# Kernel tuning notes

Hardware: AMD Instinct MI355X
Metric: run time of the kernel (lower is better)

## Reference

```python
import jax, jax.numpy as jnp
import numpy as np

N, D, E, L, H, F1, G, A = 4096, 256, 131072, 3, 4, 128, 16, 32

def setup_inputs() -> dict:
    key = jax.random.key(0)
    ks = jax.random.split(key, 12)
    s = lambda k, shape, fan: jax.random.normal(k, shape, jnp.float32) / np.sqrt(fan)
    return {
        "x": jax.random.normal(ks[0], (N, D), jnp.float32),
        "edge_attr": jax.random.uniform(ks[1], (E,), jnp.float32),
        "conv_Wself": s(ks[2], (L, D, D), D),
        "conv_Wnbr": s(ks[3], (L, D, D), D),
        "conv_b": jnp.zeros((L, D), jnp.float32),
        "bn_gamma": jnp.ones((L - 1, D), jnp.float32),
        "bn_beta": jnp.zeros((L - 1, D), jnp.float32),
        "bn_mean": jnp.zeros((L - 1, D), jnp.float32),
        "bn_var": jnp.ones((L - 1, D), jnp.float32),
        "Wqkv": s(ks[4], (3, D, D), D),
        "bqkv": jnp.zeros((3, D), jnp.float32),
        "Wo": s(ks[5], (D, D), D),
        "bo": jnp.zeros((D,), jnp.float32),
        "fc1_W": s(ks[6], (D, F1), D),
        "fc1_b": jnp.zeros((F1,), jnp.float32),
        "AW1": s(ks[7], (G, F1, A), F1),
        "Ab1": jnp.zeros((G, A), jnp.float32),
        "AW2": s(ks[8], (G, A, 1), A),
        "Ab2": jnp.zeros((G, 1), jnp.float32),
        "edge_index": jax.random.randint(ks[9], (2, E), 0, N, jnp.int32),
        "node_groups": jax.random.randint(ks[10], (N,), 0, G, jnp.int32),
    }


def reference(x, edge_attr, conv_Wself, conv_Wnbr, conv_b, bn_gamma, bn_beta,
              bn_mean, bn_var, Wqkv, bqkv, Wo, bo, fc1_W, fc1_b,
              AW1, Ab1, AW2, Ab2, edge_index, node_groups):
    src, dst = edge_index[0], edge_index[1]
    # message-passing conv stack (edge_attr only used by the last, non-attention layer)
    for i in range(L):
        msg = x[src]
        if i == L - 1:
            msg = msg * edge_attr[:, None]
        agg = jax.ops.segment_sum(msg, dst, num_segments=N)
        x = x @ conv_Wself[i] + agg @ conv_Wnbr[i] + conv_b[i]
        if i < L - 1:
            x = bn_gamma[i] * (x - bn_mean[i]) * jax.lax.rsqrt(bn_var[i] + 1e-5) + bn_beta[i]
            x = jax.nn.elu(x)
    # hierarchy self-attention over all N nodes (batch of 1), residual add
    dh = D // H
    q = (x @ Wqkv[0] + bqkv[0]).reshape(N, H, dh)
    k = (x @ Wqkv[1] + bqkv[1]).reshape(N, H, dh)
    v = (x @ Wqkv[2] + bqkv[2]).reshape(N, H, dh)
    scores = jnp.einsum('nhd,mhd->hnm', q, k) / np.sqrt(dh).astype(np.float32)
    attn = jax.nn.softmax(scores, axis=-1)
    o = jnp.einsum('hnm,mhd->nhd', attn, v).reshape(N, D) @ Wo + bo
    x = x + o
    feats = jax.nn.elu(x @ fc1_W + fc1_b)  # [N, F1]; dropout is eval no-op
    # MoE-style per-node group adapter routing: gather tiny MLP weights per node
    h = jax.nn.relu(jnp.einsum('nd,nda->na', feats, AW1[node_groups]) + Ab1[node_groups])
    out = jnp.einsum('na,nao->no', h, AW2[node_groups]) + Ab2[node_groups]  # [N, 1]
    return out
```

## Files before the change

### kernel.cpp

```cpp
#include <hip/hip_runtime.h>
#include <math.h>

#define NN   4096
#define DIM  256
#define NE   131072
#define NH   4
#define DH   64
#define F1D  128
#define NG   16
#define AD   32

typedef unsigned short u16;
typedef unsigned int   u32;
typedef _Float16 f16;
typedef __attribute__((ext_vector_type(8))) _Float16 half8;
typedef __attribute__((ext_vector_type(4))) float f32x4;

enum { EPI_BIAS = 0, EPI_BNELU = 1 };
enum { MEPI_WO = 0, MEPI_FC1 = 1 };

#define MFMA16(a, b, c) __builtin_amdgcn_mfma_f32_16x16x32_f16(a, b, c, 0, 0, 0)

__device__ inline u16 f2h(float x) { union { f16 f; u16 u; } c; c.f = (f16)x; return c.u; }
__device__ inline float h2f(u16 h) { union { f16 f; u16 u; } c; c.u = h; return (float)c.f; }
__device__ inline void split16(float x, u16& h, u16& l) {
    union { f16 f; u16 u; } ch, cl;
    ch.f = (f16)x;
    cl.f = (f16)(x - (float)ch.f);
    h = ch.u; l = cl.u;
}
__device__ inline int swz64(int row, int colByte) {
    return row * 64 + ((colByte ^ ((row & 7) << 4)) >> 1);
}

__global__ void csr_count(const int* __restrict__ dst, int* __restrict__ cnt) {
    int e = blockIdx.x * 256 + threadIdx.x;
    atomicAdd(&cnt[dst[e]], 1);
}

__global__ __launch_bounds__(1024) void csr_scan(
    int* __restrict__ cnt, int* __restrict__ off)
{
    __shared__ int wsum[16];
    const int t = threadIdx.x;
    const int lane = t & 63;
    int4 v = *(const int4*)&cnt[t * 4];
    const int s = v.x + v.y + v.z + v.w;
    int acc = s;
    #pragma unroll
    for (int o = 1; o < 64; o <<= 1) {
        int u = __shfl_up(acc, o);
        if (lane >= o) acc += u;
    }
    if (lane == 63) wsum[t >> 6] = acc;
    __syncthreads();
    if (t < 16) {
        int w0 = wsum[t];
        int a2 = w0;
        #pragma unroll
        for (int o = 1; o < 16; o <<= 1) {
            int u = __shfl_up(a2, o);
            if (t >= o) a2 += u;
        }
        wsum[t] = a2 - w0;
    }
    __syncthreads();
    const int base = wsum[t >> 6] + (acc - s);
    off[t * 4 + 0] = base;
    off[t * 4 + 1] = base + v.x;
    off[t * 4 + 2] = base + v.x + v.y;
    off[t * 4 + 3] = base + v.x + v.y + v.z;
    *(int4*)&cnt[t * 4] = make_int4(0, 0, 0, 0);
    if (t == 1023) off[NN] = base + s;
}

__global__ void csr_fill(const int* __restrict__ dst, const int* __restrict__ src,
                         const float* __restrict__ eattr, const int* __restrict__ off,
                         int* __restrict__ cur, int* __restrict__ esrc,
                         float* __restrict__ ewt) {
    int e = blockIdx.x * 256 + threadIdx.x;
    int d = dst[e];
    int pos = off[d] + atomicAdd(&cur[d], 1);
    esrc[pos] = src[e];
    ewt[pos]  = eattr[e];
}

__global__ __launch_bounds__(256) void prep_kernel(
    const float* __restrict__ x,
    const float* __restrict__ Ws, const float* __restrict__ Wn,
    const float* __restrict__ Wqkv, const float* __restrict__ Wo,
    const float* __restrict__ fc1W,
    u16* __restrict__ xh, u16* __restrict__ xl,
    u16* __restrict__ wch, u16* __restrict__ wcl,
    u16* __restrict__ w4h, u16* __restrict__ w4l,
    u16* __restrict__ f1h, u16* __restrict__ f1l,
    int* __restrict__ cur)
{
    const int b = blockIdx.x;
    const int t = threadIdx.x;
    if (b < 1024) {
        const int gid = b * 256 + t;
        const float4 v = *(const float4*)&x[(size_t)gid * 4];
        u16 h[4], l[4];
        split16(v.x, h[0], l[0]); split16(v.y, h[1], l[1]);
        split16(v.z, h[2], l[2]); split16(v.w, h[3], l[3]);
        *(uint2*)&xh[(size_t)gid * 4] =
            make_uint2((u32)h[0] | ((u32)h[1] << 16), (u32)h[2] | ((u32)h[3] << 16));
        *(uint2*)&xl[(size_t)gid * 4] =
            make_uint2((u32)l[0] | ((u32)l[1] << 16), (u32)l[2] | ((u32)l[3] << 16));
    } else if (b < 1408) {
        const int gid = (b - 1024) * 256 + t;
        const int L = gid / 32768;
        const int rem = gid % 32768;
        const int m = rem / 128;
        const int k4 = (rem % 128) * 4;
        const float* S = Ws + (size_t)L * 65536;
        const float* Nb = Wn + (size_t)L * 65536;
        u16 h[4], l[4];
        #pragma unroll
        for (int j = 0; j < 4; ++j) {
            const int k = k4 + j;
            const float v = (k < 256) ? S[(size_t)k * 256 + m]
                                      : Nb[(size_t)(k - 256) * 256 + m];
            split16(v, h[j], l[j]);
        }
        const size_t o = (size_t)L * 131072 + (size_t)m * 512 + k4;
        *(uint2*)&wch[o] = make_uint2((u32)h[0] | ((u32)h[1] << 16), (u32)h[2] | ((u32)h[3] << 16));
        *(uint2*)&wcl[o] = make_uint2((u32)l[0] | ((u32)l[1] << 16), (u32)l[2] | ((u32)l[3] << 16));
    } else if (b < 1664) {
        const int gid = (b - 1408) * 256 + t;
        const int mat = gid / 16384;
        const int rem = gid % 16384;
        const int m = rem / 64;
        const int k4 = (rem % 64) * 4;
        const float* W = (mat < 3) ? Wqkv + (size_t)mat * 65536 : Wo;
        u16 h[4], l[4];
        #pragma unroll
        for (int j = 0; j < 4; ++j)
            split16(W[(size_t)(k4 + j) * 256 + m], h[j], l[j]);
        const size_t o = (size_t)mat * 65536 + (size_t)m * 256 + k4;
        *(uint2*)&w4h[o] = make_uint2((u32)h[0] | ((u32)h[1] << 16), (u32)h[2] | ((u32)h[3] << 16));
        *(uint2*)&w4l[o] = make_uint2((u32)l[0] | ((u32)l[1] << 16), (u32)l[2] | ((u32)l[3] << 16));
    } else if (b < 1696) {
        const int gid = (b - 1664) * 256 + t;
        const int m = gid / 64;
        const int k4 = (gid % 64) * 4;
        u16 h[4], l[4];
        #pragma unroll
        for (int j = 0; j < 4; ++j)
            split16(fc1W[(size_t)(k4 + j) * F1D + m], h[j], l[j]);
        const size_t o = (size_t)m * 256 + k4;
        *(uint2*)&f1h[o] = make_uint2((u32)h[0] | ((u32)h[1] << 16), (u32)h[2] | ((u32)h[3] << 16));
        *(uint2*)&f1l[o] = make_uint2((u32)l[0] | ((u32)l[1] << 16), (u32)l[2] | ((u32)l[3] << 16));
    } else {
        const int gid = (b - 1696) * 256 + t;
        if (gid < NN / 4) *(int4*)&cur[gid * 4] = make_int4(0, 0, 0, 0);
    }
}

template<bool LAST>
__global__ __launch_bounds__(256) void agg_kernel(
    const float* __restrict__ x, const int* __restrict__ esrc,
    const float* __restrict__ ewt, const int* __restrict__ off,
    u16* __restrict__ aggh, u16* __restrict__ aggl)
{
    const int node = blockIdx.x * 4 + (threadIdx.x >> 6);
    const int lane = threadIdx.x & 63;
    const int d4 = lane * 4;
    int j = off[node];
    const int j1 = off[node + 1];
    float4 acc = make_float4(0.f, 0.f, 0.f, 0.f);
    for (; j + 4 <= j1; j += 4) {
        const int s0 = esrc[j], s1 = esrc[j + 1], s2 = esrc[j + 2], s3 = esrc[j + 3];
        const float4 x0 = *(const float4*)&x[(size_t)s0 * DIM + d4];
        const float4 x1 = *(const float4*)&x[(size_t)s1 * DIM + d4];
        const float4 x2 = *(const float4*)&x[(size_t)s2 * DIM + d4];
        const float4 x3 = *(const float4*)&x[(size_t)s3 * DIM + d4];
        const float w0 = LAST ? ewt[j]     : 1.f;
        const float w1 = LAST ? ewt[j + 1] : 1.f;
        const float w2 = LAST ? ewt[j + 2] : 1.f;
        const float w3 = LAST ? ewt[j + 3] : 1.f;
        acc.x = fmaf(x0.x, w0, acc.x); acc.y = fmaf(x0.y, w0, acc.y);
        acc.z = fmaf(x0.z, w0, acc.z); acc.w = fmaf(x0.w, w0, acc.w);
        acc.x = fmaf(x1.x, w1, acc.x); acc.y = fmaf(x1.y, w1, acc.y);
        acc.z = fmaf(x1.z, w1, acc.z); acc.w = fmaf(x1.w, w1, acc.w);
        acc.x = fmaf(x2.x, w2, acc.x); acc.y = fmaf(x2.y, w2, acc.y);
        acc.z = fmaf(x2.z, w2, acc.z); acc.w = fmaf(x2.w, w2, acc.w);
        acc.x = fmaf(x3.x, w3, acc.x); acc.y = fmaf(x3.y, w3, acc.y);
        acc.z = fmaf(x3.z, w3, acc.z); acc.w = fmaf(x3.w, w3, acc.w);
    }
    for (; j < j1; ++j) {
        const int s = esrc[j];
        const float w = LAST ? ewt[j] : 1.f;
        const float4 xv = *(const float4*)&x[(size_t)s * DIM + d4];
        acc.x = fmaf(xv.x, w, acc.x); acc.y = fmaf(xv.y, w, acc.y);
        acc.z = fmaf(xv.z, w, acc.z); acc.w = fmaf(xv.w, w, acc.w);
    }
    u16 h[4], l[4];
    split16(acc.x, h[0], l[0]); split16(acc.y, h[1], l[1]);
    split16(acc.z, h[2], l[2]); split16(acc.w, h[3], l[3]);
    *(uint2*)&aggh[(size_t)node * DIM + d4] =
        make_uint2((u32)h[0] | ((u32)h[1] << 16), (u32)h[2] | ((u32)h[3] << 16));
    *(uint2*)&aggl[(size_t)node * DIM + d4] =
        make_uint2((u32)l[0] | ((u32)l[1] << 16), (u32)l[2] | ((u32)l[3] << 16));
}

template<int EPI>
__global__ __launch_bounds__(256) void conv_mfma(
    const u16* __restrict__ xh, const u16* __restrict__ xl,
    const u16* __restrict__ gh, const u16* __restrict__ gl,
    const u16* __restrict__ bth, const u16* __restrict__ btl,
    const float* __restrict__ bias,
    const float* __restrict__ gamma, const float* __restrict__ beta,
    const float* __restrict__ bnmean, const float* __restrict__ bnvar,
    float* __restrict__ outf, u16* __restrict__ oh, u16* __restrict__ ol)
{
    __shared__ u16 lds[13824];
    u16* As_h = lds;
    u16* As_l = lds + 2304;
    u16* Bs_h = lds + 4608;
    u16* Bs_l = lds + 9216;
    #define TKP 72

    const int tid  = threadIdx.x;
    const int row0 = blockIdx.y * 32;
    const int col0 = blockIdx.x * 64;

    const int w   = tid >> 6;
    const int l15 = tid & 15, h4 = (tid & 63) >> 4;
    const int rh  = w & 1, ch = w >> 1;
    const int arow = tid >> 3, acs = (tid & 7) * 8;
    const int brow = tid & 63, bseg = tid >> 6;
    const int bc = bseg * 16;

    uint4 sah, sal, sbh0, sbh1, sbl0, sbl1;
    {
        sah = *((const uint4*)&xh[(size_t)(row0 + arow) * DIM + acs]);
        sal = *((const uint4*)&xl[(size_t)(row0 + arow) * DIM + acs]);
        const u16* pbh = bth + (size_t)(col0 + brow) * 512 + bc;
        const u16* pbl = btl + (size_t)(col0 + brow) * 512 + bc;
        sbh0 = ((const uint4*)pbh)[0]; sbh1 = ((const uint4*)pbh)[1];
        sbl0 = ((const uint4*)pbl)[0]; sbl1 = ((const uint4*)pbl)[1];
    }

    const f32x4 z4 = {0.f, 0.f, 0.f, 0.f};
    f32x4 acc[2] = {z4, z4};

    for (int kt = 0; kt < 8; ++kt) {
        *(uint4*)&As_h[arow * TKP + acs] = sah;
        *(uint4*)&As_l[arow * TKP + acs] = sal;
        *(uint4*)&Bs_h[brow * TKP + bc]     = sbh0;
        *(uint4*)&Bs_h[brow * TKP + bc + 8] = sbh1;
        *(uint4*)&Bs_l[brow * TKP + bc]     = sbl0;
        *(uint4*)&Bs_l[brow * TKP + bc + 8] = sbl1;
        if (kt + 1 < 8) {
            const int kn = kt + 1;
            const u16 *pah, *pal;
            if (kn < 4) {
                pah = xh + (size_t)(row0 + arow) * DIM + kn * 64 + acs;
                pal = xl + (size_t)(row0 + arow) * DIM + kn * 64 + acs;
            } else {
                pah = gh + (size_t)(row0 + arow) * DIM + (kn - 4) * 64 + acs;
                pal = gl + (size_t)(row0 + arow) * DIM + (kn - 4) * 64 + acs;
            }
            sah = *((const uint4*)pah);
            sal = *((const uint4*)pal);
            const u16* pbh = bth + (size_t)(col0 + brow) * 512 + kn * 64 + bc;
            const u16* pbl = btl + (size_t)(col0 + brow) * 512 + kn * 64 + bc;
            sbh0 = ((const uint4*)pbh)[0]; sbh1 = ((const uint4*)pbh)[1];
            sbl0 = ((const uint4*)pbl)[0]; sbl1 = ((const uint4*)pbl)[1];
        }
        __syncthreads();

        __builtin_amdgcn_s_setprio(1);
        #pragma unroll
        for (int kc = 0; kc < 2; ++kc) {
            const int dc = kc * 32 + h4 * 8;
            half8 afh, afl, bfh[2], bfl[2];
            afh = *(const half8*)&As_h[(rh * 16 + l15) * TKP + dc];
            afl = *(const half8*)&As_l[(rh * 16 + l15) * TKP + dc];
            #pragma unroll
            for (int bb = 0; bb < 2; ++bb) {
                const int r = ch * 32 + bb * 16 + l15;
                bfh[bb] = *(const half8*)&Bs_h[r * TKP + dc];
                bfl[bb] = *(const half8*)&Bs_l[r * TKP + dc];
            }
            #pragma unroll
            for (int bb = 0; bb < 2; ++bb) {
                acc[bb] = MFMA16(afh, bfh[bb], acc[bb]);
                acc[bb] = MFMA16(afh, bfl[bb], acc[bb]);
                acc[bb] = MFMA16(afl, bfh[bb], acc[bb]);
            }
        }
        __builtin_amdgcn_s_setprio(0);
        __syncthreads();
    }

    #pragma unroll
    for (int bb = 0; bb < 2; ++bb) {
        const int c  = col0 + ch * 32 + bb * 16 + l15;
        const int r0 = row0 + rh * 16 + h4 * 4;
        #pragma unroll
        for (int i = 0; i < 4; ++i) {
            const int r = r0 + i;
            float t = acc[bb][i] + bias[c];
            if (EPI == EPI_BNELU) {
                t = gamma[c] * (t - bnmean[c]) * rsqrtf(bnvar[c] + 1e-5f) + beta[c];
                t = t > 0.f ? t : expm1f(t);
            }
            outf[(size_t)r * DIM + c] = t;
            u16 hh, ll;
            split16(t, hh, ll);
            oh[(size_t)r * DIM + c] = hh;
            ol[(size_t)r * DIM + c] = ll;
        }
    }
    #undef TKP
}

__global__ __launch_bounds__(256) void qkv_mfma(
    const u16* __restrict__ xh, const u16* __restrict__ xl,
    const u16* __restrict__ wth, const u16* __restrict__ wtl,
    const float* __restrict__ bias,
    u16* __restrict__ qh_o, u16* __restrict__ ql_o,
    u16* __restrict__ kh_o, u16* __restrict__ kl_o,
    u16* __restrict__ vt_o)
{
    __shared__ u16 lds[4 * 4608];
    u16* As_h = lds;
    u16* As_l = lds + 4608;
    u16* Bs_h = lds + 9216;
    u16* Bs_l = lds + 13824;
    #define TKP 72

    const int tid  = threadIdx.x;
    const int row0 = blockIdx.y * 64;
    const int mat  = blockIdx.x >> 2;
    const int col0 = (blockIdx.x & 3) * 64;
    const float* biasp = bias + mat * DIM;

    const int w   = tid >> 6;
    const int l15 = tid & 15, h4 = (tid & 63) >> 4;
    const int rh  = w & 1, ch = w >> 1;
    const int lrow = tid & 63, lseg = tid >> 6;
    const int lc = lseg * 16;

    const size_t brow = (size_t)(mat * 256 + col0 + lrow) * 256;
    uint4 sah0, sah1, sal0, sal1, sbh0, sbh1, sbl0, sbl1;
    {
        const u16* pah = xh + (size_t)(row0 + lrow) * DIM + lc;
        const u16* pal = xl + (size_t)(row0 + lrow) * DIM + lc;
        sah0 = ((const uint4*)pah)[0]; sah1 = ((const uint4*)pah)[1];
        sal0 = ((const uint4*)pal)[0]; sal1 = ((const uint4*)pal)[1];
        sbh0 = ((const uint4*)(wth + brow + lc))[0]; sbh1 = ((const uint4*)(wth + brow + lc))[1];
        sbl0 = ((const uint4*)(wtl + brow + lc))[0]; sbl1 = ((const uint4*)(wtl + brow + lc))[1];
    }

    const f32x4 z4 = {0.f, 0.f, 0.f, 0.f};
    f32x4 acc[2][2] = {{z4, z4}, {z4, z4}};

    for (int kt = 0; kt < 4; ++kt) {
        *(uint4*)&As_h[lrow * TKP + lc]     = sah0;
        *(uint4*)&As_h[lrow * TKP + lc + 8] = sah1;
        *(uint4*)&As_l[lrow * TKP + lc]     = sal0;
        *(uint4*)&As_l[lrow * TKP + lc + 8] = sal1;
        *(uint4*)&Bs_h[lrow * TKP + lc]     = sbh0;
        *(uint4*)&Bs_h[lrow * TKP + lc + 8] = sbh1;
        *(uint4*)&Bs_l[lrow * TKP + lc]     = sbl0;
        *(uint4*)&Bs_l[lrow * TKP + lc + 8] = sbl1;
        if (kt + 1 < 4) {
            const int kb = (kt + 1) * 64 + lc;
            const u16* pah = xh + (size_t)(row0 + lrow) * DIM + kb;
            const u16* pal = xl + (size_t)(row0 + lrow) * DIM + kb;
            sah0 = ((const uint4*)pah)[0]; sah1 = ((const uint4*)pah)[1];
            sal0 = ((const uint4*)pal)[0]; sal1 = ((const uint4*)pal)[1];
            sbh0 = ((const uint4*)(wth + brow + kb))[0]; sbh1 = ((const uint4*)(wth + brow + kb))[1];
            sbl0 = ((const uint4*)(wtl + brow + kb))[0]; sbl1 = ((const uint4*)(wtl + brow + kb))[1];
        }
        __syncthreads();

        __builtin_amdgcn_s_setprio(1);
        #pragma unroll
        for (int kc = 0; kc < 2; ++kc) {
            const int dc = kc * 32 + h4 * 8;
            half8 afh[2], afl[2], bfh[2], bfl[2];
            #pragma unroll
            for (int ab = 0; ab < 2; ++ab) {
                const int r = rh * 32 + ab * 16 + l15;
                afh[ab] = *(const half8*)&As_h[r * TKP + dc];
                afl[ab] = *(const half8*)&As_l[r * TKP + dc];
            }
            #pragma unroll
            for (int bb = 0; bb < 2; ++bb) {
                const int r = ch * 32 + bb * 16 + l15;
                bfh[bb] = *(const half8*)&Bs_h[r * TKP + dc];
                bfl[bb] = *(const half8*)&Bs_l[r * TKP + dc];
            }
            #pragma unroll
            for (int ab = 0; ab < 2; ++ab)
                #pragma unroll
                for (int bb = 0; bb < 2; ++bb) {
                    acc[ab][bb] = MFMA16(afh[ab], bfh[bb], acc[ab][bb]);
                    acc[ab][bb] = MFMA16(afh[ab], bfl[bb], acc[ab][bb]);
                    acc[ab][bb] = MFMA16(afl[ab], bfh[bb], acc[ab][bb]);
                }
        }
        __builtin_amdgcn_s_setprio(0);
        __syncthreads();
    }

    const float s = (mat == 0) ? 0.125f : 1.0f;
    u16* oph = (mat == 0) ? qh_o : kh_o;
    u16* opl = (mat == 0) ? ql_o : kl_o;
    #pragma unroll
    for (int ab = 0; ab < 2; ++ab)
        #pragma unroll
        for (int bb = 0; bb < 2; ++bb) {
            const int c  = col0 + ch * 32 + bb * 16 + l15;
            const int r0 = row0 + rh * 32 + ab * 16 + h4 * 4;
            if (mat < 2) {
                #pragma unroll
                for (int i = 0; i < 4; ++i) {
                    const int r = r0 + i;
                    const float t = (acc[ab][bb][i] + biasp[c]) * s;
                    u16 hh, ll;
                    split16(t, hh, ll);
                    oph[(size_t)r * DIM + c] = hh;
                    opl[(size_t)r * DIM + c] = ll;
                }
            } else {
                u16 v[4];
                #pragma unroll
                for (int i = 0; i < 4; ++i)
                    v[i] = f2h(acc[ab][bb][i] + biasp[c]);
                *(uint2*)&vt_o[(size_t)c * NN + r0] =
                    make_uint2((u32)v[0] | ((u32)v[1] << 16), (u32)v[2] | ((u32)v[3] << 16));
            }
        }
    #undef TKP
}

template<int MEPI>
__global__ __launch_bounds__(256) void mfma_gemm32(
    const u16* __restrict__ Ah, const u16* __restrict__ Al,
    const u16* __restrict__ Bth, const u16* __restrict__ Btl,
    const float* __restrict__ bias, const float* __restrict__ resid,
    float* __restrict__ outf, u16* __restrict__ outh, u16* __restrict__ outl,
    int K, int M)
{
    __shared__ u16 lds[13824];
    u16* As_h = lds;
    u16* As_l = lds + 2304;
    u16* Bs_h = lds + 4608;
    u16* Bs_l = lds + 9216;
    #define TKP 72

    const int tid  = threadIdx.x;
    const int row0 = blockIdx.y * 32;
    const int col0 = blockIdx.x * 64;

    const int w   = tid >> 6;
    const int l15 = tid & 15, h4 = (tid & 63) >> 4;
    const int rh  = w & 1, ch = w >> 1;
    const int arow = tid >> 3, acs = (tid & 7) * 8;
    const int brow = tid & 63, bseg = tid >> 6;
    const int bc = bseg * 16;

    uint4 sah, sal, sbh0, sbh1, sbl0, sbl1;
    {
        sah = *((const uint4*)&Ah[(size_t)(row0 + arow) * K + acs]);
        sal = *((const uint4*)&Al[(size_t)(row0 + arow) * K + acs]);
        const u16* pbh = Bth + (size_t)(col0 + brow) * K + bc;
        const u16* pbl = Btl + (size_t)(col0 + brow) * K + bc;
        sbh0 = ((const uint4*)pbh)[0]; sbh1 = ((const uint4*)pbh)[1];
        sbl0 = ((const uint4*)pbl)[0]; sbl1 = ((const uint4*)pbl)[1];
    }

    const f32x4 z4 = {0.f, 0.f, 0.f, 0.f};
    f32x4 acc[2] = {z4, z4};
    const int NKT2 = K / 64;

    for (int kt = 0; kt < NKT2; ++kt) {
        *(uint4*)&As_h[arow * TKP + acs] = sah;
        *(uint4*)&As_l[arow * TKP + acs] = sal;
        *(uint4*)&Bs_h[brow * TKP + bc]     = sbh0;
        *(uint4*)&Bs_h[brow * TKP + bc + 8] = sbh1;
        *(uint4*)&Bs_l[brow * TKP + bc]     = sbl0;
        *(uint4*)&Bs_l[brow * TKP + bc + 8] = sbl1;
        if (kt + 1 < NKT2) {
            const int kb = (kt + 1) * 64;
            sah = *((const uint4*)&Ah[(size_t)(row0 + arow) * K + kb + acs]);
            sal = *((const uint4*)&Al[(size_t)(row0 + arow) * K + kb + acs]);
            const u16* pbh = Bth + (size_t)(col0 + brow) * K + kb + bc;
            const u16* pbl = Btl + (size_t)(col0 + brow) * K + kb + bc;
            sbh0 = ((const uint4*)pbh)[0]; sbh1 = ((const uint4*)pbh)[1];
            sbl0 = ((const uint4*)pbl)[0]; sbl1 = ((const uint4*)pbl)[1];
        }
        __syncthreads();

        __builtin_amdgcn_s_setprio(1);
        #pragma unroll
        for (int kc = 0; kc < 2; ++kc) {
            const int dc = kc * 32 + h4 * 8;
            half8 afh, afl, bfh[2], bfl[2];
            afh = *(const half8*)&As_h[(rh * 16 + l15) * TKP + dc];
            afl = *(const half8*)&As_l[(rh * 16 + l15) * TKP + dc];
            #pragma unroll
            for (int bb = 0; bb < 2; ++bb) {
                const int r = ch * 32 + bb * 16 + l15;
                bfh[bb] = *(const half8*)&Bs_h[r * TKP + dc];
                bfl[bb] = *(const half8*)&Bs_l[r * TKP + dc];
            }
            #pragma unroll
            for (int bb = 0; bb < 2; ++bb) {
                acc[bb] = MFMA16(afh, bfh[bb], acc[bb]);
                acc[bb] = MFMA16(afh, bfl[bb], acc[bb]);
                acc[bb] = MFMA16(afl, bfh[bb], acc[bb]);
            }
        }
        __builtin_amdgcn_s_setprio(0);
        __syncthreads();
    }

    #pragma unroll
    for (int bb = 0; bb < 2; ++bb) {
        const int c  = col0 + ch * 32 + bb * 16 + l15;
        const int r0 = row0 + rh * 16 + h4 * 4;
        #pragma unroll
        for (int i = 0; i < 4; ++i) {
            const int r = r0 + i;
            float t = acc[bb][i] + bias[c];
            if (MEPI == MEPI_WO) {
                t += resid[(size_t)r * M + c];
                u16 hh, ll;
                split16(t, hh, ll);
                outh[(size_t)r * M + c] = hh;
                outl[(size_t)r * M + c] = ll;
            } else {
                t = t > 0.f ? t : expm1f(t);
                outf[(size_t)r * M + c] = t;
            }
        }
    }
    #undef TKP
}

#define QB 128
#define KB 64
#define NSPLIT 6
#define NKT (NN / KB)

__global__ __launch_bounds__(512, 2) void attn_kernel(
    const u16* __restrict__ qhi, const u16* __restrict__ qlo,
    const u16* __restrict__ khi, const u16* __restrict__ klo,
    const u16* __restrict__ vT,
    u16* __restrict__ op0, u16* __restrict__ op1, u16* __restrict__ op2,
    u16* __restrict__ op3, u16* __restrict__ op4, u16* __restrict__ op5,
    float* __restrict__ mpart, float* __restrict__ lpart)
{
    __shared__ u16 lds[24576];
    u16* Kh0 = lds;
    u16* Kl0 = lds + 4096;
    u16* Vt0 = lds + 8192;
    u16* Kh1 = lds + 12288;
    u16* Kl1 = lds + 16384;
    u16* Vt1 = lds + 20480;
    u16* Qh  = lds;
    u16* Ql  = lds + 8192;

    const int tid = threadIdx.x;
    const int h   = blockIdx.y;
    const int q0  = blockIdx.x * QB;
    const int sp  = blockIdx.z;
    const int kt0 = (sp * NKT) / NSPLIT;
    const int kt1 = ((sp + 1) * NKT) / NSPLIT;

    const int w   = tid >> 6;
    const int l15 = tid & 15, h4 = (tid & 63) >> 4;
    const int lrow = tid & 63, lseg = tid >> 6;
    const int gq8 = h * DH + lseg * 8;

    {
        const int qrow = tid >> 2, qseg = tid & 3;
        const u16* s0 = qhi + (size_t)(q0 + qrow) * DIM + h * DH + qseg * 16;
        const u16* s1 = qlo + (size_t)(q0 + qrow) * DIM + h * DH + qseg * 16;
        uint4 a = ((const uint4*)s0)[0], b = ((const uint4*)s0)[1];
        uint4 c = ((const uint4*)s1)[0], d = ((const uint4*)s1)[1];
        *(uint4*)&Qh[swz64(qrow, qseg * 32)]      = a;
        *(uint4*)&Qh[swz64(qrow, qseg * 32 + 16)] = b;
        *(uint4*)&Ql[swz64(qrow, qseg * 32)]      = c;
        *(uint4*)&Ql[swz64(qrow, qseg * 32 + 16)] = d;
    }

    uint4 rk, rl, rv;
    auto load_tile = [&](int kt_ld) {
        const int key0 = kt_ld * KB;
        rk = *(const uint4*)(khi + (size_t)(key0 + lrow) * DIM + gq8);
        rl = *(const uint4*)(klo + (size_t)(key0 + lrow) * DIM + gq8);
        rv = *(const uint4*)(vT + (size_t)(h * DH + lrow) * NN + key0 + lseg * 8);
    };
    load_tile(kt0);
    __syncthreads();

    half8 qf[2][2];
    #pragma unroll
    for (int kc = 0; kc < 2; ++kc) {
        const int r = w * 16 + l15;
        const int cb = kc * 64 + h4 * 16;
        qf[kc][0] = *(const half8*)&Qh[swz64(r, cb)];
        qf[kc][1] = *(const half8*)&Ql[swz64(r, cb)];
    }
    __syncthreads();

    auto stage_to = [&](u16* Kh, u16* Kl, u16* Vt) {
        const int idx = swz64(lrow, lseg * 16);
        *(uint4*)&Kh[idx] = rk;
        *(uint4*)&Kl[idx] = rl;
        *(uint4*)&Vt[idx] = rv;
    };

    stage_to(Kh0, Kl0, Vt0);
    load_tile(kt0 + 1);
    __syncthreads();

    const f32x4 z4 = {0.f, 0.f, 0.f, 0.f};
    f32x4 oacc[4] = {z4, z4, z4, z4};
    float m_run = -3.0e38f, l_run = 0.f;
    const int sl0 = (h4 & 1) * 32 + l15;
    const int sl1 = sl0 + 16;

    auto tile_body = [&](int t, u16* Kc, u16* Lc, u16* Vc,
                         u16* Kn, u16* Ln, u16* Vn) {
        if (t + 1 < kt1) stage_to(Kn, Ln, Vn);
        if (t + 2 < kt1) load_tile(t + 2);

        f32x4 sc[4] = {z4, z4, z4, z4};
        __builtin_amdgcn_s_setprio(1);
        #pragma unroll
        for (int kc = 0; kc < 2; ++kc) {
            const int cb = kc * 64 + h4 * 16;
            half8 kfh[4], kfl[4];
            #pragma unroll
            for (int kcb = 0; kcb < 4; ++kcb) {
                const int r = kcb * 16 + l15;
                const int idx = swz64(r, cb);
                kfh[kcb] = *(const half8*)&Kc[idx];
                kfl[kcb] = *(const half8*)&Lc[idx];
            }
            #pragma unroll
            for (int kcb = 0; kcb < 4; ++kcb) {
                sc[kcb] = MFMA16(kfh[kcb], qf[kc][0], sc[kcb]);
                sc[kcb] = MFMA16(kfl[kcb], qf[kc][0], sc[kcb]);
                sc[kcb] = MFMA16(kfh[kcb], qf[kc][1], sc[kcb]);
            }
        }
        __builtin_amdgcn_s_setprio(0);

        float c0 = fmaxf(fmaxf(sc[0][0], sc[0][1]), fmaxf(sc[0][2], sc[0][3]));
        float c1 = fmaxf(fmaxf(sc[1][0], sc[1][1]), fmaxf(sc[1][2], sc[1][3]));
        float c2 = fmaxf(fmaxf(sc[2][0], sc[2][1]), fmaxf(sc[2][2], sc[2][3]));
        float c3 = fmaxf(fmaxf(sc[3][0], sc[3][1]), fmaxf(sc[3][2], sc[3][3]));
        float pm = fmaxf(fmaxf(c0, c1), fmaxf(c2, c3));
        pm = fmaxf(pm, __shfl_xor(pm, 16));
        pm = fmaxf(pm, __shfl_xor(pm, 32));

        float p[4][4];
        float base, fr = 1.f;
        int resc;
        if (__all(pm - m_run <= 8.f)) {
            base = m_run;
            resc = 0;
        } else {
            const float mnew = fmaxf(m_run, pm);
            fr = __expf(m_run - mnew);
            m_run = mnew;
            base = mnew;
            resc = 1;
        }
        #pragma unroll
        for (int kcb = 0; kcb < 4; ++kcb)
            #pragma unroll
            for (int i = 0; i < 4; ++i)
                p[kcb][i] = __expf(sc[kcb][i] - base);
        float s0s = (p[0][0] + p[0][1]) + (p[0][2] + p[0][3]);
        float s1s = (p[1][0] + p[1][1]) + (p[1][2] + p[1][3]);
        float s2s = (p[2][0] + p[2][1]) + (p[2][2] + p[2][3]);
        float s3s = (p[3][0] + p[3][1]) + (p[3][2] + p[3][3]);
        float ls = (s0s + s1s) + (s2s + s3s);
        ls += __shfl_xor(ls, 16);
        ls += __shfl_xor(ls, 32);
        if (resc) {
            l_run = l_run * fr + ls;
            #pragma unroll
            for (int db = 0; db < 4; ++db) oacc[db] *= fr;
        } else {
            l_run += ls;
        }

        u32 pk01[4], pk23[4];
        #pragma unroll
        for (int kcb = 0; kcb < 4; ++kcb) {
            pk01[kcb] = (u32)f2h(p[kcb][0]) | ((u32)f2h(p[kcb][1]) << 16);
            pk23[kcb] = (u32)f2h(p[kcb][2]) | ((u32)f2h(p[kcb][3]) << 16);
        }

        const int hiSel = h4 >> 1;
        __builtin_amdgcn_s_setprio(1);
        #pragma unroll
        for (int kc = 0; kc < 2; ++kc) {
            const u32 a0 = (u32)__shfl((int)pk01[kc * 2], sl0);
            const u32 a1 = (u32)__shfl((int)pk23[kc * 2], sl0);
            const u32 a2 = (u32)__shfl((int)pk01[kc * 2], sl1);
            const u32 a3 = (u32)__shfl((int)pk23[kc * 2], sl1);
            const u32 b0 = (u32)__shfl((int)pk01[kc * 2 + 1], sl0);
            const u32 b1 = (u32)__shfl((int)pk23[kc * 2 + 1], sl0);
            const u32 b2 = (u32)__shfl((int)pk01[kc * 2 + 1], sl1);
            const u32 b3 = (u32)__shfl((int)pk23[kc * 2 + 1], sl1);
            union { half8 v; u32 u[4]; } pf;
            pf.u[0] = hiSel ? b0 : a0;
            pf.u[1] = hiSel ? b1 : a1;
            pf.u[2] = hiSel ? b2 : a2;
            pf.u[3] = hiSel ? b3 : a3;
            const int cb = kc * 64 + h4 * 16;
            #pragma unroll
            for (int db = 0; db < 4; ++db) {
                const half8 vf = *(const half8*)&Vc[swz64(db * 16 + l15, cb)];
                oacc[db] = MFMA16(vf, pf.v, oacc[db]);
            }
        }
        __builtin_amdgcn_s_setprio(0);
        __syncthreads();
    };

    {
        u16 *Kc = Kh0, *Lc = Kl0, *Vc = Vt0;
        u16 *Kn = Kh1, *Ln = Kl1, *Vn = Vt1;
        for (int t = kt0; t < kt1; ++t) {
            tile_body(t, Kc, Lc, Vc, Kn, Ln, Vn);
            u16* tmp;
            tmp = Kc; Kc = Kn; Kn = tmp;
            tmp = Lc; Lc = Ln; Ln = tmp;
            tmp = Vc; Vc = Vn; Vn = tmp;
        }
    }

    u16* ob = (sp == 0) ? op0 : ((sp == 1) ? op1 : ((sp == 2) ? op2 :
              ((sp == 3) ? op3 : ((sp == 4) ? op4 : op5))));
    const float inv = 1.f / l_run;
    #pragma unroll
    for (int db = 0; db < 4; ++db) {
        u32 w0 = (u32)f2h(oacc[db][0] * inv) | ((u32)f2h(oacc[db][1] * inv) << 16);
        u32 w1 = (u32)f2h(oacc[db][2] * inv) | ((u32)f2h(oacc[db][3] * inv) << 16);
        *(uint2*)&ob[(size_t)(q0 + w * 16 + l15) * DIM + h * DH + db * 16 + h4 * 4] =
            make_uint2(w0, w1);
    }
    if (h4 == 0) {
        const int r = w * 16 + l15;
        mpart[((size_t)sp * NN + q0 + r) * NH + h] = m_run;
        lpart[((size_t)sp * NN + q0 + r) * NH + h] = l_run;
    }
}

__global__ __launch_bounds__(256) void attn_combine(
    const u16* __restrict__ o0, const u16* __restrict__ o1,
    const u16* __restrict__ o2, const u16* __restrict__ o3,
    const u16* __restrict__ o4, const u16* __restrict__ o5,
    const float* __restrict__ mp, const float* __restrict__ lp,
    u16* __restrict__ ohi, u16* __restrict__ olo)
{
    const int gid = blockIdx.x * 256 + threadIdx.x;
    const int row = gid >> 6;
    const int c4  = (gid & 63) * 4;
    const int h   = c4 >> 6;
    float m[6], wgt[6];
    #pragma unroll
    for (int z = 0; z < 6; ++z) m[z] = mp[((size_t)z * NN + row) * NH + h];
    float M = m[0];
    #pragma unroll
    for (int z = 1; z < 6; ++z) M = fmaxf(M, m[z]);
    float den = 0.f;
    #pragma unroll
    for (int z = 0; z < 6; ++z) {
        wgt[z] = lp[((size_t)z * NN + row) * NH + h] * __expf(m[z] - M);
        den += wgt[z];
    }
    const float inv = 1.f / den;
    const u16* ps[6] = {o0, o1, o2, o3, o4, o5};
    float r[4] = {0.f, 0.f, 0.f, 0.f};
    #pragma unroll
    for (int z = 0; z < 6; ++z) {
        const uint2 v = *(const uint2*)&ps[z][(size_t)row * DIM + c4];
        r[0] += wgt[z] * h2f((u16)(v.x & 0xffff));
        r[1] += wgt[z] * h2f((u16)(v.x >> 16));
        r[2] += wgt[z] * h2f((u16)(v.y & 0xffff));
        r[3] += wgt[z] * h2f((u16)(v.y >> 16));
    }
    u16 hh[4], ll[4];
    #pragma unroll
    for (int j = 0; j < 4; ++j) split16(r[j] * inv, hh[j], ll[j]);
    *(uint2*)&ohi[(size_t)row * DIM + c4] =
        make_uint2((u32)hh[0] | ((u32)hh[1] << 16), (u32)hh[2] | ((u32)hh[3] << 16));
    *(uint2*)&olo[(size_t)row * DIM + c4] =
        make_uint2((u32)ll[0] | ((u32)ll[1] << 16), (u32)ll[2] | ((u32)ll[3] << 16));
}

__global__ __launch_bounds__(256) void adapter_kernel(
    const float* __restrict__ feats, const int* __restrict__ grp,
    const float* __restrict__ AW1, const float* __restrict__ Ab1,
    const float* __restrict__ AW2, const float* __restrict__ Ab2,
    float* __restrict__ out)
{
    const int wv = threadIdx.x >> 6;
    const int n = blockIdx.x * 4 + wv;
    const int lane = threadIdx.x & 63;
    __shared__ float f[4][F1D];
    f[wv][lane]      = feats[(size_t)n * F1D + lane];
    f[wv][lane + 64] = feats[(size_t)n * F1D + 64 + lane];
    const int g = grp[n];
    const float* W1 = AW1 + (size_t)g * F1D * AD;
    const int a = lane & 31;
    const int half = lane >> 5;
    float hsum = 0.f;
    for (int d = 0; d < 64; ++d)
        hsum = fmaf(f[wv][half * 64 + d], W1[(half * 64 + d) * AD + a], hsum);
    hsum += __shfl_xor(hsum, 32);
    hsum = fmaxf(hsum + Ab1[g * AD + a], 0.f);
    float p = hsum * AW2[g * AD + a];
    #pragma unroll
    for (int mm = 1; mm < 32; mm <<= 1) p += __shfl_xor(p, mm);
    if (lane == 0) out[n] = p + Ab2[g];
}

extern "C" void kernel_launch(void* const* d_in, const int* in_sizes, int n_in,
                              void* d_out, int out_size, void* d_ws, size_t ws_size,
                              hipStream_t stream)
{
    const float* x_in   = (const float*)d_in[0];
    const float* eattr  = (const float*)d_in[1];
    const float* Wself  = (const float*)d_in[2];
    const float* Wnbr   = (const float*)d_in[3];
    const float* convb  = (const float*)d_in[4];
    const float* gamma  = (const float*)d_in[5];
    const float* beta   = (const float*)d_in[6];
    const float* bnmean = (const float*)d_in[7];
    const float* bnvar  = (const float*)d_in[8];
    const float* Wqkv   = (const float*)d_in[9];
    const float* bqkv   = (const float*)d_in[10];
    const float* Wo     = (const float*)d_in[11];
    const float* bo     = (const float*)d_in[12];
    const float* fc1W   = (const float*)d_in[13];
    const float* fc1b   = (const float*)d_in[14];
    const float* AW1    = (const float*)d_in[15];
    const float* Ab1    = (const float*)d_in[16];
    const float* AW2    = (const float*)d_in[17];
    const float* Ab2    = (const float*)d_in[18];
    const int*   eidx   = (const int*)d_in[19];
    const int*   grp    = (const int*)d_in[20];
    const int* srcArr = eidx;
    const int* dstArr = eidx + NE;

    float* fws = (float*)d_ws;
    const size_t NM = (size_t)NN * DIM;
    float* bufA  = fws;
    float* bufB  = fws + NM;
    float* bufC  = fws + 2 * NM;
    float* feats = fws + 3 * NM;
    float* mpart = fws + 3 * NM + NM / 2;
    float* lpart = mpart + 6 * NN * NH;
    u16* up = (u16*)(lpart + 6 * NN * NH);
    u16* xpAh = up;             u16* xpAl = xpAh + NM;
    u16* xpBh = xpAl + NM;      u16* xpBl = xpBh + NM;
    u16* aggh = xpBl + NM;      u16* aggl = aggh + NM;
    u16* qh = aggl + NM;        u16* ql = qh + NM;
    u16* kh = ql + NM;          u16* kl = kh + NM;
    u16* vt = kl + NM;
    u16* wcath = vt + NM;
    u16* wcatl = wcath + 3 * 131072;
    u16* wt4h  = wcatl + 3 * 131072;
    u16* wt4l  = wt4h + 4 * 65536;
    u16* fc1h  = wt4l + 4 * 65536;
    u16* fc1l  = fc1h + 32768;
    int*   esrc = (int*)(fc1l + 32768);
    float* ewt  = (float*)(esrc + NE);
    int* off    = (int*)(ewt + NE);
    int* cur    = off + NN + 1;
    float* outp = (float*)d_out;

    u16* o0 = (u16*)bufB;
    u16* o1 = (u16*)bufC;
    u16* o2 = xpAh;
    u16* o3 = xpBh;
    u16* o4 = aggh;
    u16* o5 = (u16*)feats;

    prep_kernel<<<1700, 256, 0, stream>>>(
        x_in, Wself, Wnbr, Wqkv, Wo, fc1W,
        xpAh, xpAl, wcath, wcatl, wt4h, wt4l, fc1h, fc1l, cur);

    csr_count<<<NE / 256, 256, 0, stream>>>(dstArr, cur);
    csr_scan<<<1, 1024, 0, stream>>>(cur, off);
    csr_fill<<<NE / 256, 256, 0, stream>>>(dstArr, srcArr, eattr, off, cur, esrc, ewt);

    const dim3 gc(DIM / 64, NN / 32);
    const int rgrid = NN * DIM / 4 / 256;

    agg_kernel<false><<<NN / 4, 256, 0, stream>>>(x_in, esrc, ewt, off, aggh, aggl);
    conv_mfma<EPI_BNELU><<<gc, 256, 0, stream>>>(
        xpAh, xpAl, aggh, aggl, wcath, wcatl, convb,
        gamma, beta, bnmean, bnvar, bufA, xpBh, xpBl);
    agg_kernel<false><<<NN / 4, 256, 0, stream>>>(bufA, esrc, ewt, off, aggh, aggl);
    conv_mfma<EPI_BNELU><<<gc, 256, 0, stream>>>(
        xpBh, xpBl, aggh, aggl, wcath + 131072, wcatl + 131072, convb + DIM,
        gamma + DIM, beta + DIM, bnmean + DIM, bnvar + DIM, bufC, xpAh, xpAl);
    agg_kernel<true><<<NN / 4, 256, 0, stream>>>(bufC, esrc, ewt, off, aggh, aggl);
    conv_mfma<EPI_BIAS><<<gc, 256, 0, stream>>>(
        xpAh, xpAl, aggh, aggl, wcath + 262144, wcatl + 262144, convb + 2 * DIM,
        nullptr, nullptr, nullptr, nullptr, bufA, xpBh, xpBl);

    qkv_mfma<<<dim3(12, NN / 64), 256, 0, stream>>>(
        xpBh, xpBl, wt4h, wt4l, bqkv, qh, ql, kh, kl, vt);

    attn_kernel<<<dim3(NN / QB, NH, NSPLIT), 512, 0, stream>>>(
        qh, ql, kh, kl, vt, o0, o1, o2, o3, o4, o5, mpart, lpart);
    attn_combine<<<rgrid, 256, 0, stream>>>(
        o0, o1, o2, o3, o4, o5, mpart, lpart, qh, ql);

    mfma_gemm32<MEPI_WO><<<dim3(DIM / 64, NN / 32), 256, 0, stream>>>(
        qh, ql, wt4h + 3 * 65536, wt4l + 3 * 65536, bo, bufA,
        nullptr, kh, kl, DIM, DIM);

    mfma_gemm32<MEPI_FC1><<<dim3(F1D / 64, NN / 32), 256, 0, stream>>>(
        kh, kl, fc1h, fc1l, fc1b, nullptr, feats, nullptr, nullptr, DIM, F1D);

    adapter_kernel<<<NN / 4, 256, 0, stream>>>(feats, grp, AW1, Ab1, AW2, Ab2, outp);
}
```

Measured before the change: 211.5 us.

## Fuse split-KV attention combine into Wo GEMM and reduce splits to four

Removes the separate attn_combine kernel: the Wo projection now reads the four partial attention outputs plus their max/sum statistics, merges them while staging A tiles into LDS, and splits the result into hi/lo halves there. The number of key splits drops from six to four, so fewer partial buffers are written and read. The cost is less parallelism in the attention kernel, and the Wo GEMM redoes the combine work for each of its four column blocks.

```diff
diff --git a/kernel.cpp b/kernel.cpp
--- a/kernel.cpp
+++ b/kernel.cpp
@@ -15,9 +15,6 @@
 typedef _Float16 f16;
 typedef __attribute__((ext_vector_type(8))) _Float16 half8;
 typedef __attribute__((ext_vector_type(4))) float f32x4;
-
-enum { EPI_BIAS = 0, EPI_BNELU = 1 };
-enum { MEPI_WO = 0, MEPI_FC1 = 1 };
 
 #define MFMA16(a, b, c) __builtin_amdgcn_mfma_f32_16x16x32_f16(a, b, c, 0, 0, 0)
 
@@ -304,7 +301,7 @@
         for (int i = 0; i < 4; ++i) {
             const int r = r0 + i;
             float t = acc[bb][i] + bias[c];
-            if (EPI == EPI_BNELU) {
+            if (EPI == 1) {
                 t = gamma[c] * (t - bnmean[c]) * rsqrtf(bnvar[c] + 1e-5f) + beta[c];
                 t = t > 0.f ? t : expm1f(t);
             }
@@ -440,13 +437,13 @@
     #undef TKP
 }
 
-template<int MEPI>
-__global__ __launch_bounds__(256) void mfma_gemm32(
-    const u16* __restrict__ Ah, const u16* __restrict__ Al,
+__global__ __launch_bounds__(256) void wo_fused(
+    const u16* __restrict__ p0, const u16* __restrict__ p1,
+    const u16* __restrict__ p2, const u16* __restrict__ p3,
+    const float* __restrict__ mp, const float* __restrict__ lp,
     const u16* __restrict__ Bth, const u16* __restrict__ Btl,
     const float* __restrict__ bias, const float* __restrict__ resid,
-    float* __restrict__ outf, u16* __restrict__ outh, u16* __restrict__ outl,
-    int K, int M)
+    u16* __restrict__ outh, u16* __restrict__ outl)
 {
     __shared__ u16 lds[13824];
     u16* As_h = lds;
@@ -454,6 +451,131 @@
     u16* Bs_h = lds + 4608;
     u16* Bs_l = lds + 9216;
     #define TKP 72
+    const int K = DIM, M = DIM;
+
+    const int tid  = threadIdx.x;
+    const int row0 = blockIdx.y * 32;
+    const int col0 = blockIdx.x * 64;
+
+    const int w   = tid >> 6;
+    const int l15 = tid & 15, h4 = (tid & 63) >> 4;
+    const int rh  = w & 1, ch = w >> 1;
+    const int arow = tid >> 3, acs = (tid & 7) * 8;
+    const int brow = tid & 63, bseg = tid >> 6;
+    const int bc = bseg * 16;
+    const int r = row0 + arow;
+
+    uint4 pa0, pa1, pa2, pa3, sbh0, sbh1, sbl0, sbl1;
+    {
+        const size_t ao = (size_t)r * DIM + acs;
+        pa0 = *(const uint4*)&p0[ao];
+        pa1 = *(const uint4*)&p1[ao];
+        pa2 = *(const uint4*)&p2[ao];
+        pa3 = *(const uint4*)&p3[ao];
+        const u16* pbh = Bth + (size_t)(col0 + brow) * K + bc;
+        const u16* pbl = Btl + (size_t)(col0 + brow) * K + bc;
+        sbh0 = ((const uint4*)pbh)[0]; sbh1 = ((const uint4*)pbh)[1];
+        sbl0 = ((const uint4*)pbl)[0]; sbl1 = ((const uint4*)pbl)[1];
+    }
+
+    const f32x4 z4 = {0.f, 0.f, 0.f, 0.f};
+    f32x4 acc[2] = {z4, z4};
+
+    for (int kt = 0; kt < 4; ++kt) {
+        {
+            const int hd = kt;
+            const float m0 = mp[((size_t)0 * NN + r) * NH + hd];
+            const float m1 = mp[((size_t)1 * NN + r) * NH + hd];
+            const float m2 = mp[((size_t)2 * NN + r) * NH + hd];
+            const float m3 = mp[((size_t)3 * NN + r) * NH + hd];
+            const float M2 = fmaxf(fmaxf(m0, m1), fmaxf(m2, m3));
+            const float w0 = lp[((size_t)0 * NN + r) * NH + hd] * __expf(m0 - M2);
+            const float w1 = lp[((size_t)1 * NN + r) * NH + hd] * __expf(m1 - M2);
+            const float w2 = lp[((size_t)2 * NN + r) * NH + hd] * __expf(m2 - M2);
+            const float w3 = lp[((size_t)3 * NN + r) * NH + hd] * __expf(m3 - M2);
+            const float inv = 1.f / (((w0 + w1) + (w2 + w3)));
+            union { uint4 v; u16 u[8]; } a0, a1, a2, a3, oh_, ol_;
+            a0.v = pa0; a1.v = pa1; a2.v = pa2; a3.v = pa3;
+            #pragma unroll
+            for (int j = 0; j < 8; ++j) {
+                const float mv = (w0 * h2f(a0.u[j]) + w1 * h2f(a1.u[j]) +
+                                  w2 * h2f(a2.u[j]) + w3 * h2f(a3.u[j])) * inv;
+                split16(mv, oh_.u[j], ol_.u[j]);
+            }
+            *(uint4*)&As_h[arow * TKP + acs] = oh_.v;
+            *(uint4*)&As_l[arow * TKP + acs] = ol_.v;
+        }
+        *(uint4*)&Bs_h[brow * TKP + bc]     = sbh0;
+        *(uint4*)&Bs_h[brow * TKP + bc + 8] = sbh1;
+        *(uint4*)&Bs_l[brow * TKP + bc]     = sbl0;
+        *(uint4*)&Bs_l[brow * TKP + bc + 8] = sbl1;
+        if (kt + 1 < 4) {
+            const size_t ao = (size_t)r * DIM + (kt + 1) * 64 + acs;
+            pa0 = *(const uint4*)&p0[ao];
+            pa1 = *(const uint4*)&p1[ao];
+            pa2 = *(const uint4*)&p2[ao];
+            pa3 = *(const uint4*)&p3[ao];
+            const int kb = (kt + 1) * 64;
+            const u16* pbh = Bth + (size_t)(col0 + brow) * K + kb + bc;
+            const u16* pbl = Btl + (size_t)(col0 + brow) * K + kb + bc;
+            sbh0 = ((const uint4*)pbh)[0]; sbh1 = ((const uint4*)pbh)[1];
+            sbl0 = ((const uint4*)pbl)[0]; sbl1 = ((const uint4*)pbl)[1];
+        }
+        __syncthreads();
+
+        __builtin_amdgcn_s_setprio(1);
+        #pragma unroll
+        for (int kc = 0; kc < 2; ++kc) {
+            const int dc = kc * 32 + h4 * 8;
+            half8 afh, afl, bfh[2], bfl[2];
+            afh = *(const half8*)&As_h[(rh * 16 + l15) * TKP + dc];
+            afl = *(const half8*)&As_l[(rh * 16 + l15) * TKP + dc];
+            #pragma unroll
+            for (int bb = 0; bb < 2; ++bb) {
+                const int rr = ch * 32 + bb * 16 + l15;
+                bfh[bb] = *(const half8*)&Bs_h[rr * TKP + dc];
+                bfl[bb] = *(const half8*)&Bs_l[rr * TKP + dc];
+            }
+            #pragma unroll
+            for (int bb = 0; bb < 2; ++bb) {
+                acc[bb] = MFMA16(afh, bfh[bb], acc[bb]);
+                acc[bb] = MFMA16(afh, bfl[bb], acc[bb]);
+                acc[bb] = MFMA16(afl, bfh[bb], acc[bb]);
+            }
+        }
+        __builtin_amdgcn_s_setprio(0);
+        __syncthreads();
+    }
+
+    #pragma unroll
+    for (int bb = 0; bb < 2; ++bb) {
+        const int c  = col0 + ch * 32 + bb * 16 + l15;
+        const int r0 = row0 + rh * 16 + h4 * 4;
+        #pragma unroll
+        for (int i = 0; i < 4; ++i) {
+            const int rr = r0 + i;
+            float t = acc[bb][i] + bias[c] + resid[(size_t)rr * M + c];
+            u16 hh, ll;
+            split16(t, hh, ll);
+            outh[(size_t)rr * M + c] = hh;
+            outl[(size_t)rr * M + c] = ll;
+        }
+    }
+    #undef TKP
+}
+
+__global__ __launch_bounds__(256) void fc1_mfma(
+    const u16* __restrict__ Ah, const u16* __restrict__ Al,
+    const u16* __restrict__ Bth, const u16* __restrict__ Btl,
+    const float* __restrict__ bias, float* __restrict__ outf)
+{
+    __shared__ u16 lds[13824];
+    u16* As_h = lds;
+    u16* As_l = lds + 2304;
+    u16* Bs_h = lds + 4608;
+    u16* Bs_l = lds + 9216;
+    #define TKP 72
+    const int K = DIM, M = F1D;
 
     const int tid  = threadIdx.x;
     const int row0 = blockIdx.y * 32;
@@ -478,16 +600,15 @@
 
     const f32x4 z4 = {0.f, 0.f, 0.f, 0.f};
     f32x4 acc[2] = {z4, z4};
-    const int NKT2 = K / 64;
-
-    for (int kt = 0; kt < NKT2; ++kt) {
+
+    for (int kt = 0; kt < 4; ++kt) {
         *(uint4*)&As_h[arow * TKP + acs] = sah;
         *(uint4*)&As_l[arow * TKP + acs] = sal;
         *(uint4*)&Bs_h[brow * TKP + bc]     = sbh0;
         *(uint4*)&Bs_h[brow * TKP + bc + 8] = sbh1;
         *(uint4*)&Bs_l[brow * TKP + bc]     = sbl0;
         *(uint4*)&Bs_l[brow * TKP + bc + 8] = sbl1;
-        if (kt + 1 < NKT2) {
+        if (kt + 1 < 4) {
             const int kb = (kt + 1) * 64;
             sah = *((const uint4*)&Ah[(size_t)(row0 + arow) * K + kb + acs]);
             sal = *((const uint4*)&Al[(size_t)(row0 + arow) * K + kb + acs]);
@@ -507,9 +628,9 @@
             afl = *(const half8*)&As_l[(rh * 16 + l15) * TKP + dc];
             #pragma unroll
             for (int bb = 0; bb < 2; ++bb) {
-                const int r = ch * 32 + bb * 16 + l15;
-                bfh[bb] = *(const half8*)&Bs_h[r * TKP + dc];
-                bfl[bb] = *(const half8*)&Bs_l[r * TKP + dc];
+                const int rr = ch * 32 + bb * 16 + l15;
+                bfh[bb] = *(const half8*)&Bs_h[rr * TKP + dc];
+                bfl[bb] = *(const half8*)&Bs_l[rr * TKP + dc];
             }
             #pragma unroll
             for (int bb = 0; bb < 2; ++bb) {
@@ -528,18 +649,10 @@
         const int r0 = row0 + rh * 16 + h4 * 4;
         #pragma unroll
         for (int i = 0; i < 4; ++i) {
-            const int r = r0 + i;
+            const int rr = r0 + i;
             float t = acc[bb][i] + bias[c];
-            if (MEPI == MEPI_WO) {
-                t += resid[(size_t)r * M + c];
-                u16 hh, ll;
-                split16(t, hh, ll);
-                outh[(size_t)r * M + c] = hh;
-                outl[(size_t)r * M + c] = ll;
-            } else {
-                t = t > 0.f ? t : expm1f(t);
-                outf[(size_t)r * M + c] = t;
-            }
+            t = t > 0.f ? t : expm1f(t);
+            outf[(size_t)rr * M + c] = t;
         }
     }
     #undef TKP
@@ -547,15 +660,15 @@
 
 #define QB 128
 #define KB 64
-#define NSPLIT 6
+#define NSPLIT 4
 #define NKT (NN / KB)
 
 __global__ __launch_bounds__(512, 2) void attn_kernel(
     const u16* __restrict__ qhi, const u16* __restrict__ qlo,
     const u16* __restrict__ khi, const u16* __restrict__ klo,
     const u16* __restrict__ vT,
-    u16* __restrict__ op0, u16* __restrict__ op1, u16* __restrict__ op2,
-    u16* __restrict__ op3, u16* __restrict__ op4, u16* __restrict__ op5,
+    u16* __restrict__ op0, u16* __restrict__ op1,
+    u16* __restrict__ op2, u16* __restrict__ op3,
     float* __restrict__ mpart, float* __restrict__ lpart)
 {
     __shared__ u16 lds[24576];
@@ -744,8 +857,7 @@
         }
     }
 
-    u16* ob = (sp == 0) ? op0 : ((sp == 1) ? op1 : ((sp == 2) ? op2 :
-              ((sp == 3) ? op3 : ((sp == 4) ? op4 : op5))));
+    u16* ob = (sp == 0) ? op0 : ((sp == 1) ? op1 : ((sp == 2) ? op2 : op3));
     const float inv = 1.f / l_run;
     #pragma unroll
     for (int db = 0; db < 4; ++db) {
@@ -759,49 +871,6 @@
         mpart[((size_t)sp * NN + q0 + r) * NH + h] = m_run;
         lpart[((size_t)sp * NN + q0 + r) * NH + h] = l_run;
     }
-}
-
-__global__ __launch_bounds__(256) void attn_combine(
-    const u16* __restrict__ o0, const u16* __restrict__ o1,
-    const u16* __restrict__ o2, const u16* __restrict__ o3,
-    const u16* __restrict__ o4, const u16* __restrict__ o5,
-    const float* __restrict__ mp, const float* __restrict__ lp,
-    u16* __restrict__ ohi, u16* __restrict__ olo)
-{
-    const int gid = blockIdx.x * 256 + threadIdx.x;
-    const int row = gid >> 6;
-    const int c4  = (gid & 63) * 4;
-    const int h   = c4 >> 6;
-    float m[6], wgt[6];
-    #pragma unroll
-    for (int z = 0; z < 6; ++z) m[z] = mp[((size_t)z * NN + row) * NH + h];
-    float M = m[0];
-    #pragma unroll
-    for (int z = 1; z < 6; ++z) M = fmaxf(M, m[z]);
-    float den = 0.f;
-    #pragma unroll
-    for (int z = 0; z < 6; ++z) {
-        wgt[z] = lp[((size_t)z * NN + row) * NH + h] * __expf(m[z] - M);
-        den += wgt[z];
-    }
-    const float inv = 1.f / den;
-    const u16* ps[6] = {o0, o1, o2, o3, o4, o5};
-    float r[4] = {0.f, 0.f, 0.f, 0.f};
-    #pragma unroll
-    for (int z = 0; z < 6; ++z) {
-        const uint2 v = *(const uint2*)&ps[z][(size_t)row * DIM + c4];
-        r[0] += wgt[z] * h2f((u16)(v.x & 0xffff));
-        r[1] += wgt[z] * h2f((u16)(v.x >> 16));
-        r[2] += wgt[z] * h2f((u16)(v.y & 0xffff));
-        r[3] += wgt[z] * h2f((u16)(v.y >> 16));
-    }
-    u16 hh[4], ll[4];
-    #pragma unroll
-    for (int j = 0; j < 4; ++j) split16(r[j] * inv, hh[j], ll[j]);
-    *(uint2*)&ohi[(size_t)row * DIM + c4] =
-        make_uint2((u32)hh[0] | ((u32)hh[1] << 16), (u32)hh[2] | ((u32)hh[3] << 16));
-    *(uint2*)&olo[(size_t)row * DIM + c4] =
-        make_uint2((u32)ll[0] | ((u32)ll[1] << 16), (u32)ll[2] | ((u32)ll[3] << 16));
 }
 
 __global__ __launch_bounds__(256) void adapter_kernel(
@@ -866,8 +935,8 @@
     float* bufC  = fws + 2 * NM;
     float* feats = fws + 3 * NM;
     float* mpart = fws + 3 * NM + NM / 2;
-    float* lpart = mpart + 6 * NN * NH;
-    u16* up = (u16*)(lpart + 6 * NN * NH);
+    float* lpart = mpart + 4 * NN * NH;
+    u16* up = (u16*)(lpart + 4 * NN * NH);
     u16* xpAh = up;             u16* xpAl = xpAh + NM;
     u16* xpBh = xpAl + NM;      u16* xpBl = xpBh + NM;
     u16* aggh = xpBl + NM;      u16* aggl = aggh + NM;
@@ -890,8 +959,6 @@
     u16* o1 = (u16*)bufC;
     u16* o2 = xpAh;
     u16* o3 = xpBh;
-    u16* o4 = aggh;
-    u16* o5 = (u16*)feats;
 
     prep_kernel<<<1700, 256, 0, stream>>>(
         x_in, Wself, Wnbr, Wqkv, Wo, fc1W,
@@ -902,18 +969,16 @@
     csr_fill<<<NE / 256, 256, 0, stream>>>(dstArr, srcArr, eattr, off, cur, esrc, ewt);
 
     const dim3 gc(DIM / 64, NN / 32);
-    const int rgrid = NN * DIM / 4 / 256;
-
     agg_kernel<false><<<NN / 4, 256, 0, stream>>>(x_in, esrc, ewt, off, aggh, aggl);
-    conv_mfma<EPI_BNELU><<<gc, 256, 0, stream>>>(
+    conv_mfma<1><<<gc, 256, 0, stream>>>(
         xpAh, xpAl, aggh, aggl, wcath, wcatl, convb,
         gamma, beta, bnmean, bnvar, bufA, xpBh, xpBl);
     agg_kernel<false><<<NN / 4, 256, 0, stream>>>(bufA, esrc, ewt, off, aggh, aggl);
-    conv_mfma<EPI_BNELU><<<gc, 256, 0, stream>>>(
+    conv_mfma<1><<<gc, 256, 0, stream>>>(
         xpBh, xpBl, aggh, aggl, wcath + 131072, wcatl + 131072, convb + DIM,
         gamma + DIM, beta + DIM, bnmean + DIM, bnvar + DIM, bufC, xpAh, xpAl);
     agg_kernel<true><<<NN / 4, 256, 0, stream>>>(bufC, esrc, ewt, off, aggh, aggl);
-    conv_mfma<EPI_BIAS><<<gc, 256, 0, stream>>>(
+    conv_mfma<0><<<gc, 256, 0, stream>>>(
         xpAh, xpAl, aggh, aggl, wcath + 262144, wcatl + 262144, convb + 2 * DIM,
         nullptr, nullptr, nullptr, nullptr, bufA, xpBh, xpBl);
 
@@ -921,16 +986,14 @@
         xpBh, xpBl, wt4h, wt4l, bqkv, qh, ql, kh, kl, vt);
 
     attn_kernel<<<dim3(NN / QB, NH, NSPLIT), 512, 0, stream>>>(
-        qh, ql, kh, kl, vt, o0, o1, o2, o3, o4, o5, mpart, lpart);
-    attn_combine<<<rgrid, 256, 0, stream>>>(
-        o0, o1, o2, o3, o4, o5, mpart, lpart, qh, ql);
-
-    mfma_gemm32<MEPI_WO><<<dim3(DIM / 64, NN / 32), 256, 0, stream>>>(
-        qh, ql, wt4h + 3 * 65536, wt4l + 3 * 65536, bo, bufA,
-        nullptr, kh, kl, DIM, DIM);
-
-    mfma_gemm32<MEPI_FC1><<<dim3(F1D / 64, NN / 32), 256, 0, stream>>>(
-        kh, kl, fc1h, fc1l, fc1b, nullptr, feats, nullptr, nullptr, DIM, F1D);
+        qh, ql, kh, kl, vt, o0, o1, o2, o3, mpart, lpart);
+
+    wo_fused<<<dim3(DIM / 64, NN / 32), 256, 0, stream>>>(
+        o0, o1, o2, o3, mpart, lpart,
+        wt4h + 3 * 65536, wt4l + 3 * 65536, bo, bufA, kh, kl);
+
+    fc1_mfma<<<dim3(F1D / 64, NN / 32), 256, 0, stream>>>(
+        kh, kl, fc1h, fc1l, fc1b, feats);
 
     adapter_kernel<<<NN / 4, 256, 0, stream>>>(feats, grp, AW1, Ab1, AW2, Ab2, outp);
 }
```

After: 206.5 us. 2.4% less time.
